# Kernel tuning notes

Hardware: AMD Instinct MI355X
Metric: run time of the kernel (lower is better)

Reference implementation:

```python
import jax, jax.numpy as jnp
import numpy as np


def _generate_planes():
    return jnp.array([[[1, 0, 0], [0, 1, 0], [0, 0, 1]],
                      [[0, 1, 0], [0, 0, 1], [1, 0, 0]],
                      [[0, 0, 1], [1, 0, 0], [0, 1, 0]]], dtype=jnp.float32)


def _grid_sample(image, optical):
    # image: [B, C, IH, IW], optical: [B, H, W, 2] in [-1, 1]
    B, C, IH, IW = image.shape
    _, H, W, _ = optical.shape
    ix = (optical[..., 0] + 1) / 2 * (IW - 1)
    iy = (optical[..., 1] + 1) / 2 * (IH - 1)
    # corner coords are non-differentiable (torch.no_grad in original)
    ix_nw = jax.lax.stop_gradient(jnp.floor(ix))
    iy_nw = jax.lax.stop_gradient(jnp.floor(iy))
    ix_se = ix_nw + 1
    iy_se = iy_nw + 1
    # bilinear weights computed with UNclamped corners (matches original order)
    w_nw = (ix_se - ix) * (iy_se - iy)
    w_ne = (ix - ix_nw) * (iy_se - iy)
    w_sw = (ix_se - ix) * (iy - iy_nw)
    w_se = (ix - ix_nw) * (iy - iy_nw)
    # clamp indices for the gathers
    cx0 = jnp.clip(ix_nw, 0, IW - 1).astype(jnp.int32)
    cy0 = jnp.clip(iy_nw, 0, IH - 1).astype(jnp.int32)
    cx1 = jnp.clip(ix_se, 0, IW - 1).astype(jnp.int32)
    cy1 = jnp.clip(iy_se, 0, IH - 1).astype(jnp.int32)
    flat = image.reshape(B, C, IH * IW)

    def gather(cy, cx):
        idx = (cy * IW + cx).reshape(B, 1, H * W)
        v = jnp.take_along_axis(flat, jnp.broadcast_to(idx, (B, C, H * W)), axis=2)
        return v.reshape(B, C, H, W)

    out = (gather(cy0, cx0) * w_nw[:, None] + gather(cy0, cx1) * w_ne[:, None]
           + gather(cy1, cx0) * w_sw[:, None] + gather(cy1, cx1) * w_se[:, None])
    return out


def _project_onto_planes(planes, coordinates):
    # planes: [P, 3, 3]; coordinates: [N, M, 3]
    N, M, _ = coordinates.shape
    P = planes.shape[0]
    inv_planes = jnp.linalg.inv(planes)  # [P, 3, 3]
    # [N, P, M, 3] @ [P, 3, 3] -> [N, P, M, 3]
    proj = jnp.einsum('nmc,pcd->npmd', coordinates, inv_planes)
    return proj.reshape(N * P, M, 3)[..., :2]


def setup_inputs() -> dict:
    key = jax.random.key(0)
    k1, k2 = jax.random.split(key)
    N, P, C, H, W = 1, 3, 32, 256, 256
    M = 524288
    plane_features = jax.random.normal(k1, (N, P, C, H, W), dtype=jnp.float32)
    coordinates = jax.random.uniform(k2, (N, M, 3), dtype=jnp.float32, minval=-1.0, maxval=1.0)
    return {
        'plane_features': plane_features,
        'coordinates': coordinates,
        'plane_axes': _generate_planes(),
        'box_warp': 2,
    }


def reference(plane_features, coordinates, plane_axes, box_warp):
    N, P, C, H, W = plane_features.shape
    _, M, _ = coordinates.shape
    feats = plane_features.reshape(N * P, C, H, W)
    coords = (2.0 / box_warp) * coordinates
    proj = _project_onto_planes(plane_axes, coords)[:, None]  # [N*P, 1, M, 2]
    sampled = _grid_sample(feats, proj)  # [N*P, C, 1, M]
    out = jnp.transpose(sampled, (0, 3, 2, 1)).reshape(N, P, M, C)
    return out
```

## Files before the change

kernel.cpp:

```cpp
#include <hip/hip_runtime.h>

#define PP 3
#define CC 32
#define HH 256
#define WW 256
#define HWP (HH * WW)

typedef float     f32x4 __attribute__((ext_vector_type(4)));
typedef _Float16  f16;
typedef _Float16  f16x4 __attribute__((ext_vector_type(4)));


__global__ __launch_bounds__(256) void tp_transpose(
        const float* __restrict__ in,
        f16* __restrict__ out,
        const float* __restrict__ axes,
        const int* __restrict__ box_warp_bits,
        float* __restrict__ inv_out) {
    if (blockIdx.x == 0 && blockIdx.y == 0 && threadIdx.x < PP) {
        const int t = threadIdx.x;
        int bits = *box_warp_bits;
        float bw;
        if (bits >= 1 && bits <= 100000) bw = (float)bits;
        else                             bw = __int_as_float(bits);
        const float* a = axes + t * 9;
        float a00 = a[0], a01 = a[1], a02 = a[2];
        float a10 = a[3], a11 = a[4], a12 = a[5];
        float a20 = a[6], a21 = a[7], a22 = a[8];
        float det = a00 * (a11 * a22 - a12 * a21)
                  - a01 * (a10 * a22 - a12 * a20)
                  + a02 * (a10 * a21 - a11 * a20);
        float s = (2.0f / bw) / det;
        float* o = inv_out + t * 9;
        o[0] = (a11 * a22 - a12 * a21) * s;
        o[1] = (a02 * a21 - a01 * a22) * s;
        o[2] = (a01 * a12 - a02 * a11) * s;
        o[3] = (a12 * a20 - a10 * a22) * s;
        o[4] = (a00 * a22 - a02 * a20) * s;
        o[5] = (a02 * a10 - a00 * a12) * s;
        o[6] = (a10 * a21 - a11 * a20) * s;
        o[7] = (a01 * a20 - a00 * a21) * s;
        o[8] = (a00 * a11 - a01 * a10) * s;
    }

    __shared__ float tile[CC][33];
    const int p   = blockIdx.y;
    const int pb  = blockIdx.x * 32;
    const int tid = threadIdx.x;

    const int j     = tid & 31;
    const int cbase = tid >> 5;
    const float* ip = in + (size_t)p * CC * HWP + pb + j;
#pragma unroll
    for (int it = 0; it < 4; ++it) {
        int c = cbase + it * 8;
        tile[c][j] = __builtin_nontemporal_load(ip + (size_t)c * HWP);
    }
    __syncthreads();

    const int c4 = tid & 7;
    const int jj = tid >> 3;
    f16x4 h;
    h.x = (f16)tile[c4 * 4 + 0][jj];
    h.y = (f16)tile[c4 * 4 + 1][jj];
    h.z = (f16)tile[c4 * 4 + 2][jj];
    h.w = (f16)tile[c4 * 4 + 3][jj];
    f16x4* op = (f16x4*)out + ((size_t)p * HWP + pb + jj) * 8 + c4;
    *op = h;
}

__global__ __launch_bounds__(256) void tp_sample(
        const float* __restrict__ coords,
        const f16x4* __restrict__ feat_t,
        const float* __restrict__ invp,
        f32x4* __restrict__ out,
        int M) {
    const int tid = threadIdx.x;
    const int c4  = tid & 7;
    const int m   = blockIdx.x * 32 + (tid >> 3);
    const int p   = blockIdx.y;
    if (m >= M) return;

    const float cx = coords[3 * m + 0];
    const float cy = coords[3 * m + 1];
    const float cz = coords[3 * m + 2];
    const float* iv = invp + p * 9;
    const float px = cx * iv[0] + cy * iv[3] + cz * iv[6];
    const float py = cx * iv[1] + cy * iv[4] + cz * iv[7];

    const float ix = (px + 1.0f) * 0.5f * (float)(WW - 1);
    const float iy = (py + 1.0f) * 0.5f * (float)(HH - 1);
    const float fx0 = floorf(ix), fy0 = floorf(iy);
    const float fx = ix - fx0, fy = iy - fy0;
    int x0 = (int)fx0, y0 = (int)fy0;
    int x1 = x0 + 1,   y1 = y0 + 1;
    x0 = min(max(x0, 0), WW - 1); x1 = min(max(x1, 0), WW - 1);
    y0 = min(max(y0, 0), HH - 1); y1 = min(max(y1, 0), HH - 1);
    const float w00 = (1.0f - fx) * (1.0f - fy);
    const float w01 = fx * (1.0f - fy);
    const float w10 = (1.0f - fx) * fy;
    const float w11 = fx * fy;

    const size_t base = (size_t)p * HWP * 8 + c4;
    const f16x4 h00 = feat_t[base + (size_t)(y0 * WW + x0) * 8];
    const f16x4 h01 = feat_t[base + (size_t)(y0 * WW + x1) * 8];
    const f16x4 h10 = feat_t[base + (size_t)(y1 * WW + x0) * 8];
    const f16x4 h11 = feat_t[base + (size_t)(y1 * WW + x1) * 8];

    const f32x4 v00 = __builtin_convertvector(h00, f32x4);
    const f32x4 v01 = __builtin_convertvector(h01, f32x4);
    const f32x4 v10 = __builtin_convertvector(h10, f32x4);
    const f32x4 v11 = __builtin_convertvector(h11, f32x4);

    f32x4 r = v00 * w00 + v01 * w01 + v10 * w10 + v11 * w11;

    __builtin_nontemporal_store(r, &out[((size_t)p * M + m) * 8 + c4]);
}

extern "C" void kernel_launch(void* const* d_in, const int* in_sizes, int n_in,
                              void* d_out, int out_size, void* d_ws, size_t ws_size,
                              hipStream_t stream) {
    const float* feats  = (const float*)d_in[0];
    const float* coords = (const float*)d_in[1];
    const float* axes   = (const float*)d_in[2];
    const int*   bw     = (const int*)d_in[3];
    const int M = in_sizes[1] / 3;

    f16*   trans = (f16*)d_ws;
    float* inv   = (float*)((char*)d_ws + (size_t)PP * HWP * CC * 2);

    tp_transpose<<<dim3(HWP / 32, PP), 256, 0, stream>>>(feats, trans, axes, bw, inv);
    tp_sample<<<dim3((M + 31) / 32, PP), 256, 0, stream>>>(
        coords, (const f16x4*)trans, inv, (f32x4*)d_out, M);
}
```

Baseline: 252.2 us.

## Split channels into two halves with separate transposed planes and sampling grid dimension

The transposed fp16 feature buffer is split into two channel halves of 16 channels, each stored as its own plane-major array, and sampling launches a third grid dimension over halves. Each gather now fetches 32-byte texel rows instead of 64, so a plane-half working set (2 MB per plane-half) is smaller and may fit caches better. The cost is that coordinates and bilinear weights are recomputed twice, and the output writes per point are split across two blocks, giving less contiguous stores. Coordinate loads are also made nontemporal.

```diff
diff --git a/kernel.cpp b/kernel.cpp
--- a/kernel.cpp
+++ b/kernel.cpp
@@ -5,6 +5,8 @@
 #define HH 256
 #define WW 256
 #define HWP (HH * WW)
+#define NH 2
+#define CH 16
 
 typedef float     f32x4 __attribute__((ext_vector_type(4)));
 typedef _Float16  f16;
@@ -60,13 +62,15 @@
 
     const int c4 = tid & 7;
     const int jj = tid >> 3;
-    f16x4 h;
-    h.x = (f16)tile[c4 * 4 + 0][jj];
-    h.y = (f16)tile[c4 * 4 + 1][jj];
-    h.z = (f16)tile[c4 * 4 + 2][jj];
-    h.w = (f16)tile[c4 * 4 + 3][jj];
-    f16x4* op = (f16x4*)out + ((size_t)p * HWP + pb + jj) * 8 + c4;
-    *op = h;
+    const int h  = c4 >> 2;
+    const int cg = c4 & 3;
+    f16x4 hv;
+    hv.x = (f16)tile[c4 * 4 + 0][jj];
+    hv.y = (f16)tile[c4 * 4 + 1][jj];
+    hv.z = (f16)tile[c4 * 4 + 2][jj];
+    hv.w = (f16)tile[c4 * 4 + 3][jj];
+    f16x4* op = (f16x4*)out + ((size_t)(h * PP + p) * HWP + pb + jj) * 4 + cg;
+    *op = hv;
 }
 
 __global__ __launch_bounds__(256) void tp_sample(
@@ -76,14 +80,15 @@
         f32x4* __restrict__ out,
         int M) {
     const int tid = threadIdx.x;
-    const int c4  = tid & 7;
-    const int m   = blockIdx.x * 32 + (tid >> 3);
+    const int l4  = tid & 3;
+    const int m   = blockIdx.x * 64 + (tid >> 2);
     const int p   = blockIdx.y;
+    const int h   = blockIdx.z;
     if (m >= M) return;
 
-    const float cx = coords[3 * m + 0];
-    const float cy = coords[3 * m + 1];
-    const float cz = coords[3 * m + 2];
+    const float cx = __builtin_nontemporal_load(coords + 3 * m + 0);
+    const float cy = __builtin_nontemporal_load(coords + 3 * m + 1);
+    const float cz = __builtin_nontemporal_load(coords + 3 * m + 2);
     const float* iv = invp + p * 9;
     const float px = cx * iv[0] + cy * iv[3] + cz * iv[6];
     const float py = cx * iv[1] + cy * iv[4] + cz * iv[7];
@@ -101,11 +106,11 @@
     const float w10 = (1.0f - fx) * fy;
     const float w11 = fx * fy;
 
-    const size_t base = (size_t)p * HWP * 8 + c4;
-    const f16x4 h00 = feat_t[base + (size_t)(y0 * WW + x0) * 8];
-    const f16x4 h01 = feat_t[base + (size_t)(y0 * WW + x1) * 8];
-    const f16x4 h10 = feat_t[base + (size_t)(y1 * WW + x0) * 8];
-    const f16x4 h11 = feat_t[base + (size_t)(y1 * WW + x1) * 8];
+    const size_t base = (size_t)(h * PP + p) * HWP * 4 + l4;
+    const f16x4 h00 = feat_t[base + (size_t)(y0 * WW + x0) * 4];
+    const f16x4 h01 = feat_t[base + (size_t)(y0 * WW + x1) * 4];
+    const f16x4 h10 = feat_t[base + (size_t)(y1 * WW + x0) * 4];
+    const f16x4 h11 = feat_t[base + (size_t)(y1 * WW + x1) * 4];
 
     const f32x4 v00 = __builtin_convertvector(h00, f32x4);
     const f32x4 v01 = __builtin_convertvector(h01, f32x4);
@@ -114,7 +119,7 @@
 
     f32x4 r = v00 * w00 + v01 * w01 + v10 * w10 + v11 * w11;
 
-    __builtin_nontemporal_store(r, &out[((size_t)p * M + m) * 8 + c4]);
+    __builtin_nontemporal_store(r, &out[((size_t)p * M + m) * 8 + h * 4 + l4]);
 }
 
 extern "C" void kernel_launch(void* const* d_in, const int* in_sizes, int n_in,
@@ -127,9 +132,9 @@
     const int M = in_sizes[1] / 3;
 
     f16*   trans = (f16*)d_ws;
-    float* inv   = (float*)((char*)d_ws + (size_t)PP * HWP * CC * 2);
+    float* inv   = (float*)((char*)d_ws + (size_t)NH * PP * HWP * CH * 2);
 
     tp_transpose<<<dim3(HWP / 32, PP), 256, 0, stream>>>(feats, trans, axes, bw, inv);
-    tp_sample<<<dim3((M + 31) / 32, PP), 256, 0, stream>>>(
+    tp_sample<<<dim3((M + 63) / 64, PP, NH), 256, 0, stream>>>(
         coords, (const f16x4*)trans, inv, (f32x4*)d_out, M);
 }
```

Measured after the change: 309.4 us. 1.23x slower.
